# Optimization experiments

Hardware: AMD Instinct MI355X
Metric: run time of the kernel (lower is better)

Reference implementation:

```python
import jax, jax.numpy as jnp
import numpy as np

N = 50000       # nodes
E = 600000      # edges (avg degree 12)
F_IN = 64       # input_bands
F_HID = 128     # 2 * input_bands
F_OUT = 128     # output_bands
EPS = 1e-5      # BatchNorm eps


def setup_inputs() -> dict:
    key = jax.random.key(0)
    ks = jax.random.split(key, 12)
    x = jax.random.normal(ks[0], (N, F_IN), jnp.float32)
    edge_index = jax.random.randint(ks[1], (2, E), 0, N, dtype=jnp.int32)
    # GCNConv weight (glorot-ish) and bias
    W1 = jax.random.normal(ks[2], (F_IN, F_HID), jnp.float32) / np.sqrt(F_IN)
    b1 = jnp.zeros((F_HID,), jnp.float32)
    gamma1 = jnp.ones((F_HID,), jnp.float32)
    beta1 = jnp.zeros((F_HID,), jnp.float32)
    # SAGEConv: lin_l (aggregated neighbors, with bias), lin_r (root, no bias)
    Wl = jax.random.normal(ks[3], (F_HID, F_OUT), jnp.float32) / np.sqrt(F_HID)
    bl = jnp.zeros((F_OUT,), jnp.float32)
    Wr = jax.random.normal(ks[4], (F_HID, F_OUT), jnp.float32) / np.sqrt(F_HID)
    gamma2 = jnp.ones((F_OUT,), jnp.float32)
    beta2 = jnp.zeros((F_OUT,), jnp.float32)
    return {"x": x, "edge_index": edge_index, "W1": W1, "b1": b1,
            "gamma1": gamma1, "beta1": beta1, "Wl": Wl, "bl": bl,
            "Wr": Wr, "gamma2": gamma2, "beta2": beta2}


def _bn_train(h, gamma, beta):
    # BatchNorm1d in training mode: biased batch stats over the node axis
    mean = h.mean(axis=0)
    var = h.var(axis=0)
    return gamma * (h - mean) * jax.lax.rsqrt(var + EPS) + beta


def _gcn_conv(x, src, dst, W, b):
    # PyG GCNConv: x' = D^{-1/2}(A + I)D^{-1/2} X W + b
    h = x @ W                                   # [N, F_HID]
    loop = jnp.arange(N, dtype=src.dtype)
    src_sl = jnp.concatenate([src, loop])       # self-loops appended
    dst_sl = jnp.concatenate([dst, loop])
    deg = jax.ops.segment_sum(jnp.ones(E + N, h.dtype), dst_sl, num_segments=N)
    dis = jnp.where(deg > 0, jax.lax.rsqrt(deg), 0.0)  # deg^{-1/2}, inf -> 0
    norm = dis[src_sl] * dis[dst_sl]            # [E+N]
    msg = h[src_sl] * norm[:, None]             # gather + scale
    return jax.ops.segment_sum(msg, dst_sl, num_segments=N) + b


def _sage_conv(x, src, dst, Wl, bl, Wr):
    # PyG SAGEConv (mean aggr): x' = lin_l(mean_{j in N(i)} x_j) + lin_r(x_i)
    cnt = jax.ops.segment_sum(jnp.ones(E, x.dtype), dst, num_segments=N)
    neigh = jax.ops.segment_sum(x[src], dst, num_segments=N)
    neigh = neigh / jnp.maximum(cnt, 1.0)[:, None]
    return neigh @ Wl + bl + x @ Wr


def reference(x, edge_index, W1, b1, gamma1, beta1, Wl, bl, Wr, gamma2, beta2):
    src, dst = edge_index[0], edge_index[1]
    h = _gcn_conv(x, src, dst, W1, b1)
    h = jax.nn.relu(_bn_train(h, gamma1, beta1))  # dropout = identity (eval)
    h = _sage_conv(h, src, dst, Wl, bl, Wr)
    h = jax.nn.relu(_bn_train(h, gamma2, beta2))
    return h
```

## Files before the change

### kernel.cpp

```cpp
#include <hip/hip_runtime.h>

#define NN 50000
#define NE 600000
#define FIN 64
#define FHID 128
#define BN_EPS 1e-5f
#define CAP 64

typedef __attribute__((ext_vector_type(8))) short short8;
typedef __attribute__((ext_vector_type(4))) float f32x4;

__device__ __forceinline__ unsigned short f2bf(float f) {
  unsigned u = __float_as_uint(f);
  return (unsigned short)((u + 0x7FFFu + ((u >> 16) & 1u)) >> 16);
}
__device__ __forceinline__ float bfs(unsigned short u) {
  return __uint_as_float(((unsigned)u) << 16);
}
__device__ __forceinline__ float bflo(unsigned v) { return __uint_as_float(v << 16); }
__device__ __forceinline__ float bfhi(unsigned v) { return __uint_as_float(v & 0xFFFF0000u); }
__device__ __forceinline__ unsigned pk2(float lo, float hi) {
  return (unsigned)f2bf(lo) | ((unsigned)f2bf(hi) << 16);
}

__global__ __launch_bounds__(256) void bucket_fill(const int* __restrict__ src,
                                                   const int* __restrict__ dst,
                                                   int* __restrict__ cnt,
                                                   int* __restrict__ csr) {
  int e = blockIdx.x * 256 + threadIdx.x;
  if (e < NE) {
    int d = dst[e];
    int p = atomicAdd(&cnt[d], 1);
    if (p < CAP) csr[(size_t)d * CAP + p] = src[e];
  }
}

__global__ __launch_bounds__(256) void scale_x(const float* __restrict__ x,
                                               const int* __restrict__ cnt,
                                               ushort4* __restrict__ xs) {
  int i = blockIdx.x * 256 + threadIdx.x;
  float4 v = ((const float4*)x)[i];
  int node = i >> 4;
  float d = rsqrtf((float)(cnt[node] + 1));
  xs[i] = make_ushort4(f2bf(v.x * d), f2bf(v.y * d), f2bf(v.z * d), f2bf(v.w * d));
}

__device__ __forceinline__ void gacc(float& a0, float& a1, float& a2, float& a3,
                                     ushort4 v) {
  a0 += bfs(v.x); a1 += bfs(v.y); a2 += bfs(v.z); a3 += bfs(v.w);
}

__global__ __launch_bounds__(256) void gcn_agg(const unsigned short* __restrict__ xs,
                                               const int* __restrict__ csr,
                                               const int* __restrict__ cnt,
                                               unsigned short* __restrict__ xa) {
  int tid = threadIdx.x;
  int node = blockIdx.x * 16 + (tid >> 4);
  int li = tid & 15;
  int deg = cnt[node];
  int degc = min(deg, CAP);
  float di = rsqrtf((float)(deg + 1));
  ushort4 sv = *(const ushort4*)(xs + (size_t)node * FIN + li * 4);
  float a0 = bfs(sv.x), a1 = bfs(sv.y), a2 = bfs(sv.z), a3 = bfs(sv.w);
  const int* cb = csr + (size_t)node * CAP;
  int e = 0;
  for (; e + 8 <= degc; e += 8) {
    int4 sA = *(const int4*)(cb + e);
    int4 sB = *(const int4*)(cb + e + 4);
    ushort4 v0 = *(const ushort4*)(xs + (size_t)sA.x * FIN + li * 4);
    ushort4 v1 = *(const ushort4*)(xs + (size_t)sA.y * FIN + li * 4);
    ushort4 v2 = *(const ushort4*)(xs + (size_t)sA.z * FIN + li * 4);
    ushort4 v3 = *(const ushort4*)(xs + (size_t)sA.w * FIN + li * 4);
    ushort4 v4 = *(const ushort4*)(xs + (size_t)sB.x * FIN + li * 4);
    ushort4 v5 = *(const ushort4*)(xs + (size_t)sB.y * FIN + li * 4);
    ushort4 v6 = *(const ushort4*)(xs + (size_t)sB.z * FIN + li * 4);
    ushort4 v7 = *(const ushort4*)(xs + (size_t)sB.w * FIN + li * 4);
    gacc(a0, a1, a2, a3, v0); gacc(a0, a1, a2, a3, v1);
    gacc(a0, a1, a2, a3, v2); gacc(a0, a1, a2, a3, v3);
    gacc(a0, a1, a2, a3, v4); gacc(a0, a1, a2, a3, v5);
    gacc(a0, a1, a2, a3, v6); gacc(a0, a1, a2, a3, v7);
  }
  for (; e + 4 <= degc; e += 4) {
    int4 sA = *(const int4*)(cb + e);
    ushort4 v0 = *(const ushort4*)(xs + (size_t)sA.x * FIN + li * 4);
    ushort4 v1 = *(const ushort4*)(xs + (size_t)sA.y * FIN + li * 4);
    ushort4 v2 = *(const ushort4*)(xs + (size_t)sA.z * FIN + li * 4);
    ushort4 v3 = *(const ushort4*)(xs + (size_t)sA.w * FIN + li * 4);
    gacc(a0, a1, a2, a3, v0); gacc(a0, a1, a2, a3, v1);
    gacc(a0, a1, a2, a3, v2); gacc(a0, a1, a2, a3, v3);
  }
  for (; e < degc; ++e) {
    ushort4 v = *(const ushort4*)(xs + (size_t)cb[e] * FIN + li * 4);
    gacc(a0, a1, a2, a3, v);
  }
  ushort4 o = make_ushort4(f2bf(di * a0), f2bf(di * a1), f2bf(di * a2), f2bf(di * a3));
  *(ushort4*)(xa + (size_t)node * FIN + li * 4) = o;
}

__device__ __forceinline__ void sacc(float* a, uint4 v) {
  a[0] += bflo(v.x); a[1] += bfhi(v.x);
  a[2] += bflo(v.y); a[3] += bfhi(v.y);
  a[4] += bflo(v.z); a[5] += bfhi(v.z);
  a[6] += bflo(v.w); a[7] += bfhi(v.w);
}

__global__ __launch_bounds__(256) void sage_agg(const unsigned* __restrict__ hb,
                                                const int* __restrict__ csr,
                                                const int* __restrict__ cnt,
                                                unsigned* __restrict__ neighb) {
  int tid = threadIdx.x;
  int node = blockIdx.x * 16 + (tid >> 4);
  int li = tid & 15;
  int deg = cnt[node];
  int degc = min(deg, CAP);
  float a[8];
#pragma unroll
  for (int i = 0; i < 8; ++i) a[i] = 0.f;
  const int* cb = csr + (size_t)node * CAP;
  int e = 0;
  for (; e + 8 <= degc; e += 8) {
    int4 sA = *(const int4*)(cb + e);
    int4 sB = *(const int4*)(cb + e + 4);
    uint4 v0 = *(const uint4*)(hb + (size_t)sA.x * 64 + li * 4);
    uint4 v1 = *(const uint4*)(hb + (size_t)sA.y * 64 + li * 4);
    uint4 v2 = *(const uint4*)(hb + (size_t)sA.z * 64 + li * 4);
    uint4 v3 = *(const uint4*)(hb + (size_t)sA.w * 64 + li * 4);
    uint4 v4 = *(const uint4*)(hb + (size_t)sB.x * 64 + li * 4);
    uint4 v5 = *(const uint4*)(hb + (size_t)sB.y * 64 + li * 4);
    uint4 v6 = *(const uint4*)(hb + (size_t)sB.z * 64 + li * 4);
    uint4 v7 = *(const uint4*)(hb + (size_t)sB.w * 64 + li * 4);
    sacc(a, v0); sacc(a, v1); sacc(a, v2); sacc(a, v3);
    sacc(a, v4); sacc(a, v5); sacc(a, v6); sacc(a, v7);
  }
  for (; e + 4 <= degc; e += 4) {
    int4 sA = *(const int4*)(cb + e);
    uint4 v0 = *(const uint4*)(hb + (size_t)sA.x * 64 + li * 4);
    uint4 v1 = *(const uint4*)(hb + (size_t)sA.y * 64 + li * 4);
    uint4 v2 = *(const uint4*)(hb + (size_t)sA.z * 64 + li * 4);
    uint4 v3 = *(const uint4*)(hb + (size_t)sA.w * 64 + li * 4);
    sacc(a, v0); sacc(a, v1); sacc(a, v2); sacc(a, v3);
  }
  for (; e < degc; ++e) {
    uint4 v = *(const uint4*)(hb + (size_t)cb[e] * 64 + li * 4);
    sacc(a, v);
  }
  float inv = 1.0f / fmaxf((float)deg, 1.0f);
  uint4 o;
  o.x = pk2(a[0] * inv, a[1] * inv);
  o.y = pk2(a[2] * inv, a[3] * inv);
  o.z = pk2(a[4] * inv, a[5] * inv);
  o.w = pk2(a[6] * inv, a[7] * inv);
  *(uint4*)(neighb + (size_t)node * 64 + li * 4) = o;
}

template <int K1, int K2, bool OUTBF>
__global__ __launch_bounds__(256) void gemm_mfma(const short* __restrict__ A1,
                                                 const short* __restrict__ A2,
                                                 const float* __restrict__ B1,
                                                 const float* __restrict__ B2,
                                                 const float* __restrict__ bias,
                                                 float* __restrict__ Cf,
                                                 unsigned short* __restrict__ Cb,
                                                 float* __restrict__ sums,
                                                 float* __restrict__ sumsq) {
  constexpr int KT = K1 + K2;
  constexpr int NK1 = K1 / 32;
  constexpr int NKS = KT / 32;
  __shared__ short Bp[8 * NKS * 64 * 8];
  __shared__ float lsum[128], lsq[128];
  int tid = threadIdx.x;
  if (tid < 128) { lsum[tid] = 0.f; lsq[tid] = 0.f; }
  for (int idx = tid; idx < KT * 32; idx += 256) {
    int k = idx >> 5, c4 = idx & 31;
    const float* Bsrc = (K2 == 0 || k < K1) ? (B1 + k * 128) : (B2 + (k - K1) * 128);
    float4 wv = *(const float4*)(Bsrc + c4 * 4);
    int ks = k >> 5, q = (k >> 3) & 3, kk = k & 7;
#pragma unroll
    for (int j = 0; j < 4; ++j) {
      int c = c4 * 4 + j;
      int nf = c >> 4, r = c & 15;
      float wj = j == 0 ? wv.x : (j == 1 ? wv.y : (j == 2 ? wv.z : wv.w));
      Bp[((nf * NKS + ks) * 64 + q * 16 + r) * 8 + kk] = (short)f2bf(wj);
    }
  }
  __syncthreads();

  int lane = tid & 63;
  int w = tid >> 6;
  int r = lane & 15;
  int q = lane >> 4;
  int row_base = blockIdx.x * 128 + w * 32;
  int row0 = row_base + r;
  int row1 = row_base + 16 + r;
  row0 = row0 < NN ? row0 : NN - 1;
  row1 = row1 < NN ? row1 : NN - 1;

  short8 af[2][NKS];
#pragma unroll
  for (int ks = 0; ks < NKS; ++ks) {
    const short* A = (K2 == 0 || ks < NK1) ? A1 : A2;
    const int Kw = (K2 == 0 || ks < NK1) ? K1 : K2;
    const int ko = ((K2 == 0 || ks < NK1) ? ks : ks - NK1) * 32;
    af[0][ks] = *(const short8*)(A + (size_t)row0 * Kw + ko + q * 8);
    af[1][ks] = *(const short8*)(A + (size_t)row1 * Kw + ko + q * 8);
  }

  f32x4 acc[2][8];
#pragma unroll
  for (int m = 0; m < 2; ++m)
#pragma unroll
    for (int n = 0; n < 8; ++n) acc[m][n] = (f32x4){0.f, 0.f, 0.f, 0.f};

#pragma unroll
  for (int ks = 0; ks < NKS; ++ks) {
#pragma unroll
    for (int n = 0; n < 8; ++n) {
      short8 bf = *(const short8*)(Bp + ((size_t)(n * NKS + ks) * 64 + lane) * 8);
      acc[0][n] = __builtin_amdgcn_mfma_f32_16x16x32_bf16(af[0][ks], bf, acc[0][n], 0, 0, 0);
      acc[1][n] = __builtin_amdgcn_mfma_f32_16x16x32_bf16(af[1][ks], bf, acc[1][n], 0, 0, 0);
    }
  }

  float bias_r[8];
#pragma unroll
  for (int n = 0; n < 8; ++n) bias_r[n] = bias[n * 16 + r];
  float cs[8], cq[8];
#pragma unroll
  for (int n = 0; n < 8; ++n) { cs[n] = 0.f; cq[n] = 0.f; }
#pragma unroll
  for (int m = 0; m < 2; ++m)
#pragma unroll
    for (int i = 0; i < 4; ++i) {
      int row = row_base + m * 16 + q * 4 + i;
      if (row < NN) {
#pragma unroll
        for (int n = 0; n < 8; ++n) {
          float v = acc[m][n][i] + bias_r[n];
          int col = n * 16 + r;
          if constexpr (OUTBF)
            Cb[(size_t)row * 128 + col] = f2bf(v);
          else
            Cf[(size_t)row * 128 + col] = v;
          cs[n] += v;
          cq[n] += v * v;
        }
      }
    }
#pragma unroll
  for (int n = 0; n < 8; ++n) {
    atomicAdd(&lsum[n * 16 + r], cs[n]);
    atomicAdd(&lsq[n * 16 + r], cq[n]);
  }
  __syncthreads();
  if (tid < 128) {
    atomicAdd(&sums[tid], lsum[tid]);
    atomicAdd(&sumsq[tid], lsq[tid]);
  }
}

__global__ __launch_bounds__(256) void bn_apply_bf(unsigned* __restrict__ hb,
                                                   const float* __restrict__ sums,
                                                   const float* __restrict__ sumsq,
                                                   const float* __restrict__ gamma,
                                                   const float* __restrict__ beta) {
  __shared__ float sc[128], sh[128];
  int t = threadIdx.x;
  if (t < 128) {
    float mean = sums[t] * (1.0f / NN);
    float var = fmaxf(sumsq[t] * (1.0f / NN) - mean * mean, 0.f);
    float inv = rsqrtf(var + BN_EPS);
    float s = gamma[t] * inv;
    sc[t] = s;
    sh[t] = beta[t] - mean * s;
  }
  __syncthreads();
  int i = blockIdx.x * 256 + t;
  uint2 v = ((uint2*)hb)[i];
  int c = (i & 31) * 4;
  float f0 = fmaxf(fmaf(bflo(v.x), sc[c + 0], sh[c + 0]), 0.f);
  float f1 = fmaxf(fmaf(bfhi(v.x), sc[c + 1], sh[c + 1]), 0.f);
  float f2 = fmaxf(fmaf(bflo(v.y), sc[c + 2], sh[c + 2]), 0.f);
  float f3 = fmaxf(fmaf(bfhi(v.y), sc[c + 3], sh[c + 3]), 0.f);
  v.x = (unsigned)f2bf(f0) | ((unsigned)f2bf(f1) << 16);
  v.y = (unsigned)f2bf(f2) | ((unsigned)f2bf(f3) << 16);
  ((uint2*)hb)[i] = v;
}

__global__ __launch_bounds__(256) void bn_apply_f32(float* __restrict__ out,
                                                    const float* __restrict__ sums,
                                                    const float* __restrict__ sumsq,
                                                    const float* __restrict__ gamma,
                                                    const float* __restrict__ beta) {
  __shared__ float sc[128], sh[128];
  int t = threadIdx.x;
  if (t < 128) {
    float mean = sums[t] * (1.0f / NN);
    float var = fmaxf(sumsq[t] * (1.0f / NN) - mean * mean, 0.f);
    float inv = rsqrtf(var + BN_EPS);
    float s = gamma[t] * inv;
    sc[t] = s;
    sh[t] = beta[t] - mean * s;
  }
  __syncthreads();
  int i4 = blockIdx.x * 256 + t;
  float4 v = ((const float4*)out)[i4];
  int f = (i4 & 31) * 4;
  v.x = fmaxf(fmaf(v.x, sc[f + 0], sh[f + 0]), 0.f);
  v.y = fmaxf(fmaf(v.y, sc[f + 1], sh[f + 1]), 0.f);
  v.z = fmaxf(fmaf(v.z, sc[f + 2], sh[f + 2]), 0.f);
  v.w = fmaxf(fmaf(v.w, sc[f + 3], sh[f + 3]), 0.f);
  ((float4*)out)[i4] = v;
}

extern "C" void kernel_launch(void* const* d_in, const int* in_sizes, int n_in,
                              void* d_out, int out_size, void* d_ws, size_t ws_size,
                              hipStream_t stream) {
  const float* x   = (const float*)d_in[0];
  const int*   ei  = (const int*)d_in[1];
  const float* W1  = (const float*)d_in[2];
  const float* b1  = (const float*)d_in[3];
  const float* g1  = (const float*)d_in[4];
  const float* be1 = (const float*)d_in[5];
  const float* Wl  = (const float*)d_in[6];
  const float* bl  = (const float*)d_in[7];
  const float* Wr  = (const float*)d_in[8];
  const float* g2  = (const float*)d_in[9];
  const float* be2 = (const float*)d_in[10];
  const int* srcp = ei;
  const int* dstp = ei + NE;

  char* w = (char*)d_ws;
  auto alloc = [&](size_t bytes) {
    char* p = w;
    w += (bytes + 255) & ~(size_t)255;
    return p;
  };
  int*   cnt     = (int*)alloc((size_t)NN * 4);
  int*   csr     = (int*)alloc((size_t)NN * CAP * 4);
  unsigned short* xs     = (unsigned short*)alloc((size_t)NN * FIN * 2);
  unsigned short* xa     = (unsigned short*)alloc((size_t)NN * FIN * 2);
  unsigned short* hb     = (unsigned short*)alloc((size_t)NN * FHID * 2);
  unsigned*       neighb = (unsigned*)alloc((size_t)NN * FHID * 2);
  float* stats   = (float*)alloc(8 * 128 * 4);
  float* sums1 = stats,       *sumsq1 = stats + 128;
  float* sums2 = stats + 512, *sumsq2 = stats + 640;

  hipMemsetAsync(cnt, 0, (size_t)NN * 4, stream);
  hipMemsetAsync(stats, 0, 8 * 128 * 4, stream);

  int nbE = (NE + 255) / 256;
  int nbA = NN / 16;
  int nbG = (NN + 127) / 128;

  bucket_fill<<<nbE, 256, 0, stream>>>(srcp, dstp, cnt, csr);
  scale_x<<<NN * FIN / 4 / 256, 256, 0, stream>>>(x, cnt, (ushort4*)xs);

  gcn_agg<<<nbA, 256, 0, stream>>>(xs, csr, cnt, xa);
  gemm_mfma<64, 0, true><<<nbG, 256, 0, stream>>>(
      (const short*)xa, nullptr, W1, nullptr, b1, nullptr, hb, sums1, sumsq1);
  bn_apply_bf<<<NN * FHID / 4 / 256, 256, 0, stream>>>((unsigned*)hb, sums1, sumsq1,
                                                       g1, be1);

  sage_agg<<<nbA, 256, 0, stream>>>((const unsigned*)hb, csr, cnt, neighb);
  gemm_mfma<128, 128, false><<<nbG, 256, 0, stream>>>(
      (const short*)neighb, (const short*)hb, Wl, Wr, bl, (float*)d_out, nullptr,
      sums2, sumsq2);
  bn_apply_f32<<<NN * FHID / 4 / 256, 256, 0, stream>>>((float*)d_out, sums2, sumsq2,
                                                        g2, be2);
}
```

Before: 238.5 us.

## Pad CSR rows to multiples of eight and prefetch neighbor indices in aggregation

Each node's CSR bucket is padded with zeros up to a multiple of eight, so the gather loops in gcn_agg and sage_agg use a single 8-wide body with no remainder loops. The extra contributions from padding are removed by subtracting the count times row 0's value. The next index block is software-prefetched to overlap index loads with the feature gathers. bucket_fill now processes four edges per thread with vectorized int4 loads. The padding gathers add redundant reads of row 0, and the subtraction introduces small bf16 rounding differences.

```diff
diff --git a/kernel.cpp b/kernel.cpp
--- a/kernel.cpp
+++ b/kernel.cpp
@@ -27,22 +27,33 @@
                                                    const int* __restrict__ dst,
                                                    int* __restrict__ cnt,
                                                    int* __restrict__ csr) {
-  int e = blockIdx.x * 256 + threadIdx.x;
-  if (e < NE) {
-    int d = dst[e];
-    int p = atomicAdd(&cnt[d], 1);
-    if (p < CAP) csr[(size_t)d * CAP + p] = src[e];
+  int e4 = blockIdx.x * 256 + threadIdx.x;
+  if (e4 * 4 < NE) {
+    int4 d4 = ((const int4*)dst)[e4];
+    int4 s4 = ((const int4*)src)[e4];
+    int p;
+    p = atomicAdd(&cnt[d4.x], 1); if (p < CAP) csr[(size_t)d4.x * CAP + p] = s4.x;
+    p = atomicAdd(&cnt[d4.y], 1); if (p < CAP) csr[(size_t)d4.y * CAP + p] = s4.y;
+    p = atomicAdd(&cnt[d4.z], 1); if (p < CAP) csr[(size_t)d4.z * CAP + p] = s4.z;
+    p = atomicAdd(&cnt[d4.w], 1); if (p < CAP) csr[(size_t)d4.w * CAP + p] = s4.w;
   }
 }
 
 __global__ __launch_bounds__(256) void scale_x(const float* __restrict__ x,
                                                const int* __restrict__ cnt,
-                                               ushort4* __restrict__ xs) {
+                                               ushort4* __restrict__ xs,
+                                               int* __restrict__ csr) {
   int i = blockIdx.x * 256 + threadIdx.x;
   float4 v = ((const float4*)x)[i];
   int node = i >> 4;
   float d = rsqrtf((float)(cnt[node] + 1));
   xs[i] = make_ushort4(f2bf(v.x * d), f2bf(v.y * d), f2bf(v.z * d), f2bf(v.w * d));
+  if (i < NN) {
+    int deg = min(cnt[i], CAP);
+    int deg8 = (deg + 7) & ~7;
+    int* cb = csr + (size_t)i * CAP;
+    for (int p = deg; p < deg8; ++p) cb[p] = 0;
+  }
 }
 
 __device__ __forceinline__ void gacc(float& a0, float& a1, float& a2, float& a3,
@@ -57,16 +68,20 @@
   int tid = threadIdx.x;
   int node = blockIdx.x * 16 + (tid >> 4);
   int li = tid & 15;
-  int deg = cnt[node];
-  int degc = min(deg, CAP);
-  float di = rsqrtf((float)(deg + 1));
+  int degr = cnt[node];
+  int deg = min(degr, CAP);
+  int deg8 = (deg + 7) & ~7;
+  float di = rsqrtf((float)(degr + 1));
   ushort4 sv = *(const ushort4*)(xs + (size_t)node * FIN + li * 4);
   float a0 = bfs(sv.x), a1 = bfs(sv.y), a2 = bfs(sv.z), a3 = bfs(sv.w);
+  ushort4 zv = *(const ushort4*)(xs + li * 4);
   const int* cb = csr + (size_t)node * CAP;
-  int e = 0;
-  for (; e + 8 <= degc; e += 8) {
-    int4 sA = *(const int4*)(cb + e);
-    int4 sB = *(const int4*)(cb + e + 4);
+  int4 sA = *(const int4*)(cb);
+  int4 sB = *(const int4*)(cb + 4);
+  for (int e = 0; e < deg8; e += 8) {
+    int pn = min(e + 8, CAP - 8);
+    int4 nA = *(const int4*)(cb + pn);
+    int4 nB = *(const int4*)(cb + pn + 4);
     ushort4 v0 = *(const ushort4*)(xs + (size_t)sA.x * FIN + li * 4);
     ushort4 v1 = *(const ushort4*)(xs + (size_t)sA.y * FIN + li * 4);
     ushort4 v2 = *(const ushort4*)(xs + (size_t)sA.z * FIN + li * 4);
@@ -79,20 +94,11 @@
     gacc(a0, a1, a2, a3, v2); gacc(a0, a1, a2, a3, v3);
     gacc(a0, a1, a2, a3, v4); gacc(a0, a1, a2, a3, v5);
     gacc(a0, a1, a2, a3, v6); gacc(a0, a1, a2, a3, v7);
-  }
-  for (; e + 4 <= degc; e += 4) {
-    int4 sA = *(const int4*)(cb + e);
-    ushort4 v0 = *(const ushort4*)(xs + (size_t)sA.x * FIN + li * 4);
-    ushort4 v1 = *(const ushort4*)(xs + (size_t)sA.y * FIN + li * 4);
-    ushort4 v2 = *(const ushort4*)(xs + (size_t)sA.z * FIN + li * 4);
-    ushort4 v3 = *(const ushort4*)(xs + (size_t)sA.w * FIN + li * 4);
-    gacc(a0, a1, a2, a3, v0); gacc(a0, a1, a2, a3, v1);
-    gacc(a0, a1, a2, a3, v2); gacc(a0, a1, a2, a3, v3);
-  }
-  for (; e < degc; ++e) {
-    ushort4 v = *(const ushort4*)(xs + (size_t)cb[e] * FIN + li * 4);
-    gacc(a0, a1, a2, a3, v);
-  }
+    sA = nA; sB = nB;
+  }
+  float pc = (float)(deg8 - deg);
+  a0 -= pc * bfs(zv.x); a1 -= pc * bfs(zv.y);
+  a2 -= pc * bfs(zv.z); a3 -= pc * bfs(zv.w);
   ushort4 o = make_ushort4(f2bf(di * a0), f2bf(di * a1), f2bf(di * a2), f2bf(di * a3));
   *(ushort4*)(xa + (size_t)node * FIN + li * 4) = o;
 }
@@ -111,16 +117,20 @@
   int tid = threadIdx.x;
   int node = blockIdx.x * 16 + (tid >> 4);
   int li = tid & 15;
-  int deg = cnt[node];
-  int degc = min(deg, CAP);
+  int degr = cnt[node];
+  int deg = min(degr, CAP);
+  int deg8 = (deg + 7) & ~7;
   float a[8];
 #pragma unroll
   for (int i = 0; i < 8; ++i) a[i] = 0.f;
+  uint4 zv = *(const uint4*)(hb + li * 4);
   const int* cb = csr + (size_t)node * CAP;
-  int e = 0;
-  for (; e + 8 <= degc; e += 8) {
-    int4 sA = *(const int4*)(cb + e);
-    int4 sB = *(const int4*)(cb + e + 4);
+  int4 sA = *(const int4*)(cb);
+  int4 sB = *(const int4*)(cb + 4);
+  for (int e = 0; e < deg8; e += 8) {
+    int pn = min(e + 8, CAP - 8);
+    int4 nA = *(const int4*)(cb + pn);
+    int4 nB = *(const int4*)(cb + pn + 4);
     uint4 v0 = *(const uint4*)(hb + (size_t)sA.x * 64 + li * 4);
     uint4 v1 = *(const uint4*)(hb + (size_t)sA.y * 64 + li * 4);
     uint4 v2 = *(const uint4*)(hb + (size_t)sA.z * 64 + li * 4);
@@ -131,20 +141,14 @@
     uint4 v7 = *(const uint4*)(hb + (size_t)sB.w * 64 + li * 4);
     sacc(a, v0); sacc(a, v1); sacc(a, v2); sacc(a, v3);
     sacc(a, v4); sacc(a, v5); sacc(a, v6); sacc(a, v7);
-  }
-  for (; e + 4 <= degc; e += 4) {
-    int4 sA = *(const int4*)(cb + e);
-    uint4 v0 = *(const uint4*)(hb + (size_t)sA.x * 64 + li * 4);
-    uint4 v1 = *(const uint4*)(hb + (size_t)sA.y * 64 + li * 4);
-    uint4 v2 = *(const uint4*)(hb + (size_t)sA.z * 64 + li * 4);
-    uint4 v3 = *(const uint4*)(hb + (size_t)sA.w * 64 + li * 4);
-    sacc(a, v0); sacc(a, v1); sacc(a, v2); sacc(a, v3);
-  }
-  for (; e < degc; ++e) {
-    uint4 v = *(const uint4*)(hb + (size_t)cb[e] * 64 + li * 4);
-    sacc(a, v);
-  }
-  float inv = 1.0f / fmaxf((float)deg, 1.0f);
+    sA = nA; sB = nB;
+  }
+  float pc = (float)(deg8 - deg);
+  a[0] -= pc * bflo(zv.x); a[1] -= pc * bfhi(zv.x);
+  a[2] -= pc * bflo(zv.y); a[3] -= pc * bfhi(zv.y);
+  a[4] -= pc * bflo(zv.z); a[5] -= pc * bfhi(zv.z);
+  a[6] -= pc * bflo(zv.w); a[7] -= pc * bfhi(zv.w);
+  float inv = 1.0f / fmaxf((float)degr, 1.0f);
   uint4 o;
   o.x = pk2(a[0] * inv, a[1] * inv);
   o.y = pk2(a[2] * inv, a[3] * inv);
@@ -348,12 +352,12 @@
   hipMemsetAsync(cnt, 0, (size_t)NN * 4, stream);
   hipMemsetAsync(stats, 0, 8 * 128 * 4, stream);
 
-  int nbE = (NE + 255) / 256;
+  int nbE4 = (NE / 4 + 255) / 256;
   int nbA = NN / 16;
   int nbG = (NN + 127) / 128;
 
-  bucket_fill<<<nbE, 256, 0, stream>>>(srcp, dstp, cnt, csr);
-  scale_x<<<NN * FIN / 4 / 256, 256, 0, stream>>>(x, cnt, (ushort4*)xs);
+  bucket_fill<<<nbE4, 256, 0, stream>>>(srcp, dstp, cnt, csr);
+  scale_x<<<NN * FIN / 4 / 256, 256, 0, stream>>>(x, cnt, (ushort4*)xs, csr);
 
   gcn_agg<<<nbA, 256, 0, stream>>>(xs, csr, cnt, xa);
   gemm_mfma<64, 0, true><<<nbG, 256, 0, stream>>>(
```

After: 234.6 us. No clear change (-1.7%).
